# Kernel tuning notes

Measured on AMD Instinct MI355X. Metric: run time of the kernel, lower is better.

Reference implementation:

```python
import jax, jax.numpy as jnp
import numpy as np

N_NODES = 50000
N_EDGES = 800000
N_GRAPHS = 256
D_IN, D_H1, D_H2, D_OUT = 64, 64, 64, 64


def gcn_conv(x, W, b, src, dst, n_nodes):
    # PyG GCNConv (eval): h = x @ W; add self-loops; deg[i] = in_deg(i) + 1;
    # out[i] = sum_{j->i} h[j] * deg[i]^-1/2 deg[j]^-1/2 + h[i]/deg[i] + b
    h = x @ W  # [N, F]
    ones = jnp.ones((src.shape[0],), dtype=x.dtype)
    deg = jax.ops.segment_sum(ones, dst, num_segments=n_nodes) + 1.0  # self loop
    dinv = jax.lax.rsqrt(deg)
    norm = dinv[src] * dinv[dst]  # [E]
    msg = h[src] * norm[:, None]  # [E, F]  (memory-bound gather)
    agg = jax.ops.segment_sum(msg, dst, num_segments=n_nodes)  # scatter-add
    agg = agg + h * (1.0 / deg)[:, None]  # self-loop contribution
    return agg + b


def setup_inputs() -> dict:
    key = jax.random.key(0)
    ks = jax.random.split(key, 12)
    x = jax.random.normal(ks[0], (N_NODES, D_IN), dtype=jnp.float32)
    src = jax.random.randint(ks[1], (N_EDGES,), 0, N_NODES)
    dst = jax.random.randint(ks[2], (N_EDGES,), 0, N_NODES)
    batch = jnp.sort(jax.random.randint(ks[3], (N_NODES,), 0, N_GRAPHS))
    def glorot(k, fin, fout):
        s = jnp.sqrt(6.0 / (fin + fout))
        return jax.random.uniform(k, (fin, fout), jnp.float32, -s, s)
    return {
        "x": x, "src": src, "dst": dst, "batch": batch,
        "W1": glorot(ks[4], D_IN, D_H1), "b1": jnp.zeros((D_H1,), jnp.float32),
        "W2": glorot(ks[5], D_H1, D_H2), "b2": jnp.zeros((D_H2,), jnp.float32),
        "W3": glorot(ks[6], D_H2, D_OUT), "b3": jnp.zeros((D_OUT,), jnp.float32),
        "Wl": glorot(ks[7], D_OUT, 1), "bl": jnp.zeros((1,), jnp.float32),
    }


def reference(x, src, dst, batch, W1, b1, W2, b2, W3, b3, Wl, bl):
    n = x.shape[0]
    h = jax.nn.relu(gcn_conv(x, W1, b1, src, dst, n))   # dropout inactive (eval)
    h = jax.nn.relu(gcn_conv(h, W2, b2, src, dst, n))
    h = jax.nn.relu(gcn_conv(h, W3, b3, src, dst, n))
    # global_mean_pool over graph ids
    sums = jax.ops.segment_sum(h, batch, num_segments=N_GRAPHS)  # [G, F]
    cnt = jax.ops.segment_sum(jnp.ones((n,), h.dtype), batch, num_segments=N_GRAPHS)
    pooled = sums / jnp.maximum(cnt, 1.0)[:, None]
    return pooled @ Wl + bl  # [G, 1]
```

## Files before the change

kernel.cpp:

```cpp
#include <hip/hip_runtime.h>

#define N_NODES 50000
#define N_EDGES 800000
#define N_GRAPHS 256
#define F 64
#define NBUCK 196
#define CAP 5120
#define P3_TILE 2048
#define P3_GRID ((N_EDGES + P3_TILE - 1) / P3_TILE)
#define BCAP 6144
#define ZOFF (N_NODES * 128)

__device__ __forceinline__ unsigned short f2bf(float f) {
    union { float f; unsigned u; } c; c.f = f;
    unsigned u = c.u + 0x7FFFu + ((c.u >> 16) & 1u);
    return (unsigned short)(u >> 16);
}
__device__ __forceinline__ unsigned pack2bf(float lo, float hi) {
    return (unsigned)f2bf(lo) | ((unsigned)f2bf(hi) << 16);
}
__device__ __forceinline__ float bfl(unsigned u) {
    union { unsigned u; float f; } c; c.u = u << 16; return c.f;
}
__device__ __forceinline__ float bfh(unsigned u) {
    union { unsigned u; float f; } c; c.u = u & 0xFFFF0000u; return c.f;
}

__global__ __launch_bounds__(256) void partition_edges(const int* __restrict__ src,
                                                       const int* __restrict__ dst,
                                                       int* __restrict__ bcur,
                                                       unsigned int* __restrict__ bpair) {
    __shared__ int bh[NBUCK], bloc[NBUCK], bpos[NBUCK];
    int t = threadIdx.x;
    int lo = blockIdx.x * P3_TILE;
    int hi = min(lo + P3_TILE, N_EDGES);
    for (int i = t; i < NBUCK; i += 256) { bh[i] = 0; bpos[i] = 0; }
    __syncthreads();
    for (int e = lo + t; e < hi; e += 256) atomicAdd(&bh[dst[e] >> 8], 1);
    __syncthreads();
    for (int i = t; i < NBUCK; i += 256)
        bloc[i] = bh[i] ? atomicAdd(&bcur[i], bh[i]) : 0;
    __syncthreads();
    for (int e = lo + t; e < hi; e += 256) {
        int d = dst[e];
        int b = d >> 8;
        int r = atomicAdd(&bpos[b], 1);
        bpair[(size_t)b * CAP + bloc[b] + r] = ((unsigned)src[e] << 8) | (unsigned)(d & 255);
    }
}

__global__ __launch_bounds__(256) void bucket_sort(const unsigned int* __restrict__ bpair,
                                                   const int* __restrict__ bcur,
                                                   int* __restrict__ eidx,
                                                   int* __restrict__ rbeg,
                                                   int* __restrict__ rend,
                                                   float* __restrict__ dinv,
                                                   unsigned short* __restrict__ Abf) {
    __shared__ int cnt[256], s[256], pos[256];
    __shared__ int lout[BCAP];
    int b = blockIdx.x, t = threadIdx.x;
    int base = b * CAP;
    int sz = bcur[b];

    if (b == 0 && t < 8) ((uint4*)Abf)[(size_t)N_NODES * 8 + t] = make_uint4(0u, 0u, 0u, 0u);

    cnt[t] = 0;
    __syncthreads();
    for (int i = t; i < sz; i += 256) atomicAdd(&cnt[bpair[base + i] & 255], 1);
    __syncthreads();
    int v = cnt[t];
    int pv = (v + 3) & ~3;
    s[t] = pv;
    __syncthreads();
    for (int off = 1; off < 256; off <<= 1) {
        int u = (t >= off) ? s[t - off] : 0;
        __syncthreads();
        s[t] += u;
        __syncthreads();
    }
    int excl = s[t] - pv;
    pos[t] = excl;
    int node = b * 256 + t;
    if (node < N_NODES) {
        rbeg[node] = base + excl;
        rend[node] = base + excl + pv;
        dinv[node] = 1.0f / sqrtf((float)v + 1.0f);
    }
    int padtot = s[255];
    __syncthreads();

    for (int i = t; i < sz; i += 256) {
        unsigned p = bpair[base + i];
        int r = atomicAdd(&pos[p & 255], 1);
        lout[r] = (int)((p >> 8) << 7);
    }
    __syncthreads();
    for (int j = v; j < pv; j++) lout[excl + j] = ZOFF;
    __syncthreads();
    for (int i = t; i < padtot; i += 256) eidx[base + i] = lout[i];
}

#define XSTRIDE 17
template <bool BF16IN>
__global__ __launch_bounds__(256) void gemm64_t(const void* __restrict__ Xv,
                                                const float* __restrict__ W,
                                                const float* __restrict__ dinv,
                                                unsigned short* __restrict__ Hn, int n) {
    __shared__ float4 sW[64 * 16];
    __shared__ float4 sX[128 * XSTRIDE];
    int tid = threadIdx.x;
    int base = blockIdx.x * 128;

    const float4* W4 = (const float4*)W;
    for (int i = tid; i < 64 * 16; i += 256) sW[i] = W4[i];
    if (BF16IN) {
        const uint4* X4 = (const uint4*)Xv;
        for (int i = tid; i < 128 * 8; i += 256) {
            int r = i >> 3, c = i & 7;
            int node = base + r;
            uint4 u = (node < n) ? X4[(size_t)node * 8 + c]
                                 : make_uint4(0u, 0u, 0u, 0u);
            sX[r * XSTRIDE + 2 * c]     = make_float4(bfl(u.x), bfh(u.x), bfl(u.y), bfh(u.y));
            sX[r * XSTRIDE + 2 * c + 1] = make_float4(bfl(u.z), bfh(u.z), bfl(u.w), bfh(u.w));
        }
    } else {
        const float4* X4 = (const float4*)Xv;
        for (int i = tid; i < 128 * 16; i += 256) {
            int r = i >> 4, kg = i & 15;
            int node = base + r;
            sX[r * XSTRIDE + kg] = (node < n) ? X4[(size_t)node * 16 + kg]
                                              : make_float4(0.f, 0.f, 0.f, 0.f);
        }
    }
    __syncthreads();

    int fg = tid & 15;
    int ng = tid >> 4;
    float4 acc[8];
#pragma unroll
    for (int ii = 0; ii < 8; ii++) acc[ii] = make_float4(0.f, 0.f, 0.f, 0.f);

    for (int kg = 0; kg < 16; kg++) {
        float4 xv[8];
#pragma unroll
        for (int ii = 0; ii < 8; ii++) xv[ii] = sX[(ng + 16 * ii) * XSTRIDE + kg];
#pragma unroll
        for (int kk = 0; kk < 4; kk++) {
            float4 wv = sW[(4 * kg + kk) * 16 + fg];
#pragma unroll
            for (int ii = 0; ii < 8; ii++) {
                float xs = (kk == 0) ? xv[ii].x : (kk == 1) ? xv[ii].y
                         : (kk == 2) ? xv[ii].z : xv[ii].w;
                acc[ii].x += wv.x * xs;
                acc[ii].y += wv.y * xs;
                acc[ii].z += wv.z * xs;
                acc[ii].w += wv.w * xs;
            }
        }
    }

    ushort4* H4 = (ushort4*)Hn;
#pragma unroll
    for (int ii = 0; ii < 8; ii++) {
        int node = base + ng + 16 * ii;
        if (node < n) {
            float d = dinv[node];
            float4 o = acc[ii];
            ushort4 u;
            u.x = f2bf(o.x * d); u.y = f2bf(o.y * d);
            u.z = f2bf(o.z * d); u.w = f2bf(o.w * d);
            H4[(size_t)node * 16 + fg] = u;
        }
    }
}

__global__ __launch_bounds__(256) void gather_layer(const int* __restrict__ rbeg,
                                                    const int* __restrict__ rend,
                                                    const int* __restrict__ eidx,
                                                    const float* __restrict__ dinv,
                                                    const unsigned short* __restrict__ Hn,
                                                    const float* __restrict__ b,
                                                    unsigned short* __restrict__ OUT, int n) {
    int wv = (blockIdx.x * blockDim.x + threadIdx.x) >> 6;
    int lane = threadIdx.x & 63;
    int ns = lane >> 3, f = lane & 7;
    int node = wv * 8 + ns;
    bool valid = node < n;
    int beg = valid ? rbeg[node] : 0;
    int end = valid ? rend[node] : 0;
    const char* Hb = (const char*)Hn;

    float a0 = 0.f, a1 = 0.f, a2 = 0.f, a3 = 0.f;
    float a4 = 0.f, a5 = 0.f, a6 = 0.f, a7 = 0.f;
    for (int k = beg; k < end; k += 4) {
        int4 o = *(const int4*)(eidx + k);
        uint4 p = *(const uint4*)(Hb + o.x + f * 16);
        uint4 q = *(const uint4*)(Hb + o.y + f * 16);
        uint4 r = *(const uint4*)(Hb + o.z + f * 16);
        uint4 w = *(const uint4*)(Hb + o.w + f * 16);
        a0 += (bfl(p.x) + bfl(q.x)) + (bfl(r.x) + bfl(w.x));
        a1 += (bfh(p.x) + bfh(q.x)) + (bfh(r.x) + bfh(w.x));
        a2 += (bfl(p.y) + bfl(q.y)) + (bfl(r.y) + bfl(w.y));
        a3 += (bfh(p.y) + bfh(q.y)) + (bfh(r.y) + bfh(w.y));
        a4 += (bfl(p.z) + bfl(q.z)) + (bfl(r.z) + bfl(w.z));
        a5 += (bfh(p.z) + bfh(q.z)) + (bfh(r.z) + bfh(w.z));
        a6 += (bfl(p.w) + bfl(q.w)) + (bfl(r.w) + bfl(w.w));
        a7 += (bfh(p.w) + bfh(q.w)) + (bfh(r.w) + bfh(w.w));
    }

    if (valid) {
        float di = dinv[node];
        uint4 hs = *(const uint4*)(Hb + (size_t)node * 128 + f * 16);
        float4 b0 = ((const float4*)b)[2 * f];
        float4 b1 = ((const float4*)b)[2 * f + 1];
        float v0 = fmaxf(di * (a0 + bfl(hs.x)) + b0.x, 0.f);
        float v1 = fmaxf(di * (a1 + bfh(hs.x)) + b0.y, 0.f);
        float v2 = fmaxf(di * (a2 + bfl(hs.y)) + b0.z, 0.f);
        float v3 = fmaxf(di * (a3 + bfh(hs.y)) + b0.w, 0.f);
        float v4 = fmaxf(di * (a4 + bfl(hs.z)) + b1.x, 0.f);
        float v5 = fmaxf(di * (a5 + bfh(hs.z)) + b1.y, 0.f);
        float v6 = fmaxf(di * (a6 + bfl(hs.w)) + b1.z, 0.f);
        float v7 = fmaxf(di * (a7 + bfh(hs.w)) + b1.w, 0.f);
        uint4 u;
        u.x = pack2bf(v0, v1); u.y = pack2bf(v2, v3);
        u.z = pack2bf(v4, v5); u.w = pack2bf(v6, v7);
        ((uint4*)OUT)[(size_t)node * 8 + f] = u;
    }
}

__global__ __launch_bounds__(256) void gather_pool(const int* __restrict__ rbeg,
                                                   const int* __restrict__ rend,
                                                   const int* __restrict__ eidx,
                                                   const float* __restrict__ dinv,
                                                   const unsigned short* __restrict__ Hn,
                                                   const float* __restrict__ b,
                                                   const float* __restrict__ Wl,
                                                   float* __restrict__ pdot, int n) {
    int wv = (blockIdx.x * blockDim.x + threadIdx.x) >> 6;
    int lane = threadIdx.x & 63;
    int ns = lane >> 3, f = lane & 7;
    int node = wv * 8 + ns;
    bool valid = node < n;
    int beg = valid ? rbeg[node] : 0;
    int end = valid ? rend[node] : 0;
    const char* Hb = (const char*)Hn;

    float a0 = 0.f, a1 = 0.f, a2 = 0.f, a3 = 0.f;
    float a4 = 0.f, a5 = 0.f, a6 = 0.f, a7 = 0.f;
    for (int k = beg; k < end; k += 4) {
        int4 o = *(const int4*)(eidx + k);
        uint4 p = *(const uint4*)(Hb + o.x + f * 16);
        uint4 q = *(const uint4*)(Hb + o.y + f * 16);
        uint4 r = *(const uint4*)(Hb + o.z + f * 16);
        uint4 w = *(const uint4*)(Hb + o.w + f * 16);
        a0 += (bfl(p.x) + bfl(q.x)) + (bfl(r.x) + bfl(w.x));
        a1 += (bfh(p.x) + bfh(q.x)) + (bfh(r.x) + bfh(w.x));
        a2 += (bfl(p.y) + bfl(q.y)) + (bfl(r.y) + bfl(w.y));
        a3 += (bfh(p.y) + bfh(q.y)) + (bfh(r.y) + bfh(w.y));
        a4 += (bfl(p.z) + bfl(q.z)) + (bfl(r.z) + bfl(w.z));
        a5 += (bfh(p.z) + bfh(q.z)) + (bfh(r.z) + bfh(w.z));
        a6 += (bfl(p.w) + bfl(q.w)) + (bfl(r.w) + bfl(w.w));
        a7 += (bfh(p.w) + bfh(q.w)) + (bfh(r.w) + bfh(w.w));
    }

    float di = valid ? dinv[node] : 0.f;
    uint4 hs = valid ? *(const uint4*)(Hb + (size_t)node * 128 + f * 16)
                     : make_uint4(0u, 0u, 0u, 0u);
    float4 b0 = ((const float4*)b)[2 * f];
    float4 b1 = ((const float4*)b)[2 * f + 1];
    float4 w0 = ((const float4*)Wl)[2 * f];
    float4 w1 = ((const float4*)Wl)[2 * f + 1];
    float d = 0.f;
    d += fmaxf(di * (a0 + bfl(hs.x)) + b0.x, 0.f) * w0.x;
    d += fmaxf(di * (a1 + bfh(hs.x)) + b0.y, 0.f) * w0.y;
    d += fmaxf(di * (a2 + bfl(hs.y)) + b0.z, 0.f) * w0.z;
    d += fmaxf(di * (a3 + bfh(hs.y)) + b0.w, 0.f) * w0.w;
    d += fmaxf(di * (a4 + bfl(hs.z)) + b1.x, 0.f) * w1.x;
    d += fmaxf(di * (a5 + bfh(hs.z)) + b1.y, 0.f) * w1.y;
    d += fmaxf(di * (a6 + bfl(hs.w)) + b1.z, 0.f) * w1.z;
    d += fmaxf(di * (a7 + bfh(hs.w)) + b1.w, 0.f) * w1.w;
#pragma unroll
    for (int m = 1; m <= 4; m <<= 1) d += __shfl_xor(d, m);
    if (valid && f == 0) pdot[node] = d;
}

__global__ __launch_bounds__(64) void final_out(const float* __restrict__ pdot,
                                                const int* __restrict__ batch,
                                                const float* __restrict__ bl,
                                                float* __restrict__ out) {
    int g = blockIdx.x;
    __shared__ int slo, shi;
    int lane = threadIdx.x;
    if (lane == 0) {
        int a = 0, b = N_NODES;
        while (a < b) { int m = (a + b) >> 1; if (batch[m] < g) a = m + 1; else b = m; }
        slo = a;
        b = N_NODES;
        while (a < b) { int m = (a + b) >> 1; if (batch[m] < g + 1) a = m + 1; else b = m; }
        shi = a;
    }
    __syncthreads();
    int lo = slo, hi = shi;
    float acc = 0.f;
    for (int i = lo + lane; i < hi; i += 64) acc += pdot[i];
#pragma unroll
    for (int off = 32; off > 0; off >>= 1) acc += __shfl_down(acc, off);
    if (lane == 0) {
        float cnt = (float)(hi - lo);
        out[g] = acc / fmaxf(cnt, 1.0f) + bl[0];
    }
}

extern "C" void kernel_launch(void* const* d_in, const int* in_sizes, int n_in,
                              void* d_out, int out_size, void* d_ws, size_t ws_size,
                              hipStream_t stream) {
    const float* x     = (const float*)d_in[0];
    const int*   src   = (const int*)d_in[1];
    const int*   dst   = (const int*)d_in[2];
    const int*   batch = (const int*)d_in[3];
    const float* W1 = (const float*)d_in[4];  const float* b1 = (const float*)d_in[5];
    const float* W2 = (const float*)d_in[6];  const float* b2 = (const float*)d_in[7];
    const float* W3 = (const float*)d_in[8];  const float* b3 = (const float*)d_in[9];
    const float* Wl = (const float*)d_in[10]; const float* bl = (const float*)d_in[11];
    float* out = (float*)d_out;

    char* ws = (char*)d_ws;
    unsigned short* Abf = (unsigned short*)ws;
    unsigned short* Bbf = Abf + (size_t)(N_NODES + 1) * F;
    float* dinv    = (float*)(Bbf + (size_t)N_NODES * F);
    float* pdot    = dinv + N_NODES;
    int*   rbeg    = (int*)(pdot + N_NODES);
    int*   rend    = rbeg + N_NODES;
    int*   bcur    = rend + N_NODES;
    unsigned int* bpair = (unsigned int*)(bcur + NBUCK);
    int*   eidx    = (int*)(bpair + (size_t)NBUCK * CAP);

    const int GEMM_GRID   = (N_NODES + 127) / 128;
    const int GATHER_GRID = (N_NODES + 31) / 32;

    hipMemsetAsync(bcur, 0, NBUCK * sizeof(int), stream);
    partition_edges<<<P3_GRID, 256, 0, stream>>>(src, dst, bcur, bpair);
    bucket_sort<<<NBUCK, 256, 0, stream>>>(bpair, bcur, eidx, rbeg, rend, dinv, Abf);

    gemm64_t<false><<<GEMM_GRID, 256, 0, stream>>>((const void*)x, W1, dinv, Abf, N_NODES);
    gather_layer<<<GATHER_GRID, 256, 0, stream>>>(rbeg, rend, eidx, dinv, Abf, b1, Bbf, N_NODES);

    gemm64_t<true><<<GEMM_GRID, 256, 0, stream>>>((const void*)Bbf, W2, dinv, Abf, N_NODES);
    gather_layer<<<GATHER_GRID, 256, 0, stream>>>(rbeg, rend, eidx, dinv, Abf, b2, Bbf, N_NODES);

    gemm64_t<true><<<GEMM_GRID, 256, 0, stream>>>((const void*)Bbf, W3, dinv, Abf, N_NODES);
    gather_pool<<<GATHER_GRID, 256, 0, stream>>>(rbeg, rend, eidx, dinv, Abf, b3, Wl, pdot, N_NODES);

    final_out<<<N_GRAPHS, 64, 0, stream>>>(pdot, batch, bl, out);
}
```

Measured before the change: 209.2 us.

## Fuse next-layer GEMM into gather kernel epilogue via shared memory

Each aggregation kernel now keeps its 32 output rows in shared memory after bias and ReLU, multiplies them by the next layer's weight matrix, and writes the pre-scaled bf16 features for the next gather directly. This drops two standalone GEMM launches and the bf16 round trip of intermediate activations through global memory. Buffers are ping-ponged, so the second buffer gets its own zero padding row and the workspace layout shifts. In exchange every gather block loads the 16 KB weight tile and adds a block-wide barrier, which can limit occupancy and latency hiding in the gather loop.

```diff
diff --git a/kernel.cpp b/kernel.cpp
--- a/kernel.cpp
+++ b/kernel.cpp
@@ -55,14 +55,18 @@
                                                    int* __restrict__ rbeg,
                                                    int* __restrict__ rend,
                                                    float* __restrict__ dinv,
-                                                   unsigned short* __restrict__ Abf) {
+                                                   unsigned short* __restrict__ Abf,
+                                                   unsigned short* __restrict__ Bbf) {
     __shared__ int cnt[256], s[256], pos[256];
     __shared__ int lout[BCAP];
     int b = blockIdx.x, t = threadIdx.x;
     int base = b * CAP;
     int sz = bcur[b];
 
-    if (b == 0 && t < 8) ((uint4*)Abf)[(size_t)N_NODES * 8 + t] = make_uint4(0u, 0u, 0u, 0u);
+    if (b == 0 && t < 8) {
+        ((uint4*)Abf)[(size_t)N_NODES * 8 + t] = make_uint4(0u, 0u, 0u, 0u);
+        ((uint4*)Bbf)[(size_t)N_NODES * 8 + t] = make_uint4(0u, 0u, 0u, 0u);
+    }
 
     cnt[t] = 0;
     __syncthreads();
@@ -101,11 +105,10 @@
 }
 
 #define XSTRIDE 17
-template <bool BF16IN>
-__global__ __launch_bounds__(256) void gemm64_t(const void* __restrict__ Xv,
-                                                const float* __restrict__ W,
-                                                const float* __restrict__ dinv,
-                                                unsigned short* __restrict__ Hn, int n) {
+__global__ __launch_bounds__(256) void gemm64_f32(const float* __restrict__ X,
+                                                  const float* __restrict__ W,
+                                                  const float* __restrict__ dinv,
+                                                  unsigned short* __restrict__ Hn, int n) {
     __shared__ float4 sW[64 * 16];
     __shared__ float4 sX[128 * XSTRIDE];
     int tid = threadIdx.x;
@@ -113,24 +116,12 @@
 
     const float4* W4 = (const float4*)W;
     for (int i = tid; i < 64 * 16; i += 256) sW[i] = W4[i];
-    if (BF16IN) {
-        const uint4* X4 = (const uint4*)Xv;
-        for (int i = tid; i < 128 * 8; i += 256) {
-            int r = i >> 3, c = i & 7;
-            int node = base + r;
-            uint4 u = (node < n) ? X4[(size_t)node * 8 + c]
-                                 : make_uint4(0u, 0u, 0u, 0u);
-            sX[r * XSTRIDE + 2 * c]     = make_float4(bfl(u.x), bfh(u.x), bfl(u.y), bfh(u.y));
-            sX[r * XSTRIDE + 2 * c + 1] = make_float4(bfl(u.z), bfh(u.z), bfl(u.w), bfh(u.w));
-        }
-    } else {
-        const float4* X4 = (const float4*)Xv;
-        for (int i = tid; i < 128 * 16; i += 256) {
-            int r = i >> 4, kg = i & 15;
-            int node = base + r;
-            sX[r * XSTRIDE + kg] = (node < n) ? X4[(size_t)node * 16 + kg]
-                                              : make_float4(0.f, 0.f, 0.f, 0.f);
-        }
+    const float4* X4 = (const float4*)X;
+    for (int i = tid; i < 128 * 16; i += 256) {
+        int r = i >> 4, kg = i & 15;
+        int node = base + r;
+        sX[r * XSTRIDE + kg] = (node < n) ? X4[(size_t)node * 16 + kg]
+                                          : make_float4(0.f, 0.f, 0.f, 0.f);
     }
     __syncthreads();
 
@@ -174,21 +165,29 @@
     }
 }
 
-__global__ __launch_bounds__(256) void gather_layer(const int* __restrict__ rbeg,
-                                                    const int* __restrict__ rend,
-                                                    const int* __restrict__ eidx,
-                                                    const float* __restrict__ dinv,
-                                                    const unsigned short* __restrict__ Hn,
-                                                    const float* __restrict__ b,
-                                                    unsigned short* __restrict__ OUT, int n) {
-    int wv = (blockIdx.x * blockDim.x + threadIdx.x) >> 6;
-    int lane = threadIdx.x & 63;
+__global__ __launch_bounds__(256) void gather_gemm(const int* __restrict__ rbeg,
+                                                   const int* __restrict__ rend,
+                                                   const int* __restrict__ eidx,
+                                                   const float* __restrict__ dinv,
+                                                   const unsigned short* __restrict__ HnIn,
+                                                   const float* __restrict__ b,
+                                                   const float* __restrict__ Wn,
+                                                   unsigned short* __restrict__ HnOut, int n) {
+    __shared__ float4 sW[64 * 16];
+    __shared__ float sH[32 * 68];
+    int t = threadIdx.x;
+
+    const float4* W4 = (const float4*)Wn;
+    for (int i = t; i < 64 * 16; i += 256) sW[i] = W4[i];
+
+    int wave = t >> 6, lane = t & 63;
     int ns = lane >> 3, f = lane & 7;
-    int node = wv * 8 + ns;
+    int nl = wave * 8 + ns;
+    int node = blockIdx.x * 32 + nl;
     bool valid = node < n;
     int beg = valid ? rbeg[node] : 0;
     int end = valid ? rend[node] : 0;
-    const char* Hb = (const char*)Hn;
+    const char* Hb = (const char*)HnIn;
 
     float a0 = 0.f, a1 = 0.f, a2 = 0.f, a3 = 0.f;
     float a4 = 0.f, a5 = 0.f, a6 = 0.f, a7 = 0.f;
@@ -208,23 +207,54 @@
         a7 += (bfh(p.w) + bfh(q.w)) + (bfh(r.w) + bfh(w.w));
     }
 
-    if (valid) {
-        float di = dinv[node];
-        uint4 hs = *(const uint4*)(Hb + (size_t)node * 128 + f * 16);
-        float4 b0 = ((const float4*)b)[2 * f];
-        float4 b1 = ((const float4*)b)[2 * f + 1];
-        float v0 = fmaxf(di * (a0 + bfl(hs.x)) + b0.x, 0.f);
-        float v1 = fmaxf(di * (a1 + bfh(hs.x)) + b0.y, 0.f);
-        float v2 = fmaxf(di * (a2 + bfl(hs.y)) + b0.z, 0.f);
-        float v3 = fmaxf(di * (a3 + bfh(hs.y)) + b0.w, 0.f);
-        float v4 = fmaxf(di * (a4 + bfl(hs.z)) + b1.x, 0.f);
-        float v5 = fmaxf(di * (a5 + bfh(hs.z)) + b1.y, 0.f);
-        float v6 = fmaxf(di * (a6 + bfl(hs.w)) + b1.z, 0.f);
-        float v7 = fmaxf(di * (a7 + bfh(hs.w)) + b1.w, 0.f);
-        uint4 u;
-        u.x = pack2bf(v0, v1); u.y = pack2bf(v2, v3);
-        u.z = pack2bf(v4, v5); u.w = pack2bf(v6, v7);
-        ((uint4*)OUT)[(size_t)node * 8 + f] = u;
+    float di = valid ? dinv[node] : 0.f;
+    uint4 hs = valid ? *(const uint4*)(Hb + (size_t)node * 128 + f * 16)
+                     : make_uint4(0u, 0u, 0u, 0u);
+    float4 b0 = ((const float4*)b)[2 * f];
+    float4 b1 = ((const float4*)b)[2 * f + 1];
+    float4 v0, v1;
+    v0.x = fmaxf(di * (a0 + bfl(hs.x)) + b0.x, 0.f);
+    v0.y = fmaxf(di * (a1 + bfh(hs.x)) + b0.y, 0.f);
+    v0.z = fmaxf(di * (a2 + bfl(hs.y)) + b0.z, 0.f);
+    v0.w = fmaxf(di * (a3 + bfh(hs.y)) + b0.w, 0.f);
+    v1.x = fmaxf(di * (a4 + bfl(hs.z)) + b1.x, 0.f);
+    v1.y = fmaxf(di * (a5 + bfh(hs.z)) + b1.y, 0.f);
+    v1.z = fmaxf(di * (a6 + bfl(hs.w)) + b1.z, 0.f);
+    v1.w = fmaxf(di * (a7 + bfh(hs.w)) + b1.w, 0.f);
+    float4* hdst = (float4*)&sH[nl * 68 + 8 * f];
+    hdst[0] = v0;
+    hdst[1] = v1;
+    __syncthreads();
+
+    int fg = t & 15;
+    int ng = t >> 4;
+    float4 acc0 = make_float4(0.f, 0.f, 0.f, 0.f);
+    float4 acc1 = make_float4(0.f, 0.f, 0.f, 0.f);
+    for (int k = 0; k < 64; k++) {
+        float4 wv = sW[k * 16 + fg];
+        float x0 = sH[ng * 68 + k];
+        float x1 = sH[(ng + 16) * 68 + k];
+        acc0.x += wv.x * x0; acc0.y += wv.y * x0;
+        acc0.z += wv.z * x0; acc0.w += wv.w * x0;
+        acc1.x += wv.x * x1; acc1.y += wv.y * x1;
+        acc1.z += wv.z * x1; acc1.w += wv.w * x1;
+    }
+    ushort4* H4 = (ushort4*)HnOut;
+    int n0 = blockIdx.x * 32 + ng;
+    int n1 = n0 + 16;
+    if (n0 < n) {
+        float d = dinv[n0];
+        ushort4 u;
+        u.x = f2bf(acc0.x * d); u.y = f2bf(acc0.y * d);
+        u.z = f2bf(acc0.z * d); u.w = f2bf(acc0.w * d);
+        H4[(size_t)n0 * 16 + fg] = u;
+    }
+    if (n1 < n) {
+        float d = dinv[n1];
+        ushort4 u;
+        u.x = f2bf(acc1.x * d); u.y = f2bf(acc1.y * d);
+        u.z = f2bf(acc1.z * d); u.w = f2bf(acc1.w * d);
+        H4[(size_t)n1 * 16 + fg] = u;
     }
 }
 
@@ -327,7 +357,7 @@
     char* ws = (char*)d_ws;
     unsigned short* Abf = (unsigned short*)ws;
     unsigned short* Bbf = Abf + (size_t)(N_NODES + 1) * F;
-    float* dinv    = (float*)(Bbf + (size_t)N_NODES * F);
+    float* dinv    = (float*)(Bbf + (size_t)(N_NODES + 1) * F);
     float* pdot    = dinv + N_NODES;
     int*   rbeg    = (int*)(pdot + N_NODES);
     int*   rend    = rbeg + N_NODES;
@@ -340,16 +370,15 @@
 
     hipMemsetAsync(bcur, 0, NBUCK * sizeof(int), stream);
     partition_edges<<<P3_GRID, 256, 0, stream>>>(src, dst, bcur, bpair);
-    bucket_sort<<<NBUCK, 256, 0, stream>>>(bpair, bcur, eidx, rbeg, rend, dinv, Abf);
-
-    gemm64_t<false><<<GEMM_GRID, 256, 0, stream>>>((const void*)x, W1, dinv, Abf, N_NODES);
-    gather_layer<<<GATHER_GRID, 256, 0, stream>>>(rbeg, rend, eidx, dinv, Abf, b1, Bbf, N_NODES);
-
-    gemm64_t<true><<<GEMM_GRID, 256, 0, stream>>>((const void*)Bbf, W2, dinv, Abf, N_NODES);
-    gather_layer<<<GATHER_GRID, 256, 0, stream>>>(rbeg, rend, eidx, dinv, Abf, b2, Bbf, N_NODES);
-
-    gemm64_t<true><<<GEMM_GRID, 256, 0, stream>>>((const void*)Bbf, W3, dinv, Abf, N_NODES);
-    gather_pool<<<GATHER_GRID, 256, 0, stream>>>(rbeg, rend, eidx, dinv, Abf, b3, Wl, pdot, N_NODES);
+    bucket_sort<<<NBUCK, 256, 0, stream>>>(bpair, bcur, eidx, rbeg, rend, dinv, Abf, Bbf);
+
+    gemm64_f32<<<GEMM_GRID, 256, 0, stream>>>(x, W1, dinv, Abf, N_NODES);
+
+    gather_gemm<<<GATHER_GRID, 256, 0, stream>>>(rbeg, rend, eidx, dinv, Abf, b1, W2, Bbf, N_NODES);
+
+    gather_gemm<<<GATHER_GRID, 256, 0, stream>>>(rbeg, rend, eidx, dinv, Bbf, b2, W3, Abf, N_NODES);
+
+    gather_pool<<<GATHER_GRID * 8 / 8, 256, 0, stream>>>(rbeg, rend, eidx, dinv, Abf, b3, Wl, pdot, N_NODES);
 
     final_out<<<N_GRAPHS, 64, 0, stream>>>(pdot, batch, bl, out);
 }
```

New measurement: 266.8 us. 27.6% more time.
